# Performance work log

Measured on AMD Instinct MI355X. Metric: run time of the kernel, lower is better.

The kernel has to match this reference:

```python
import jax, jax.numpy as jnp
import numpy as np

BS, D_IN, D_H, D_Z = 4096, 784, 400, 20


def setup_inputs() -> dict:
    key = jax.random.key(0)
    ks = jax.random.split(key, 13)
    s = 0.05
    return {
        "x": jax.random.normal(ks[0], (BS, D_IN), dtype=jnp.float32),
        "W1": jax.random.normal(ks[1], (D_H, D_IN), dtype=jnp.float32) * s,
        "b1": jax.random.normal(ks[2], (D_H,), dtype=jnp.float32) * s,
        "W21": jax.random.normal(ks[3], (D_Z, D_H), dtype=jnp.float32) * s,
        "b21": jax.random.normal(ks[4], (D_Z,), dtype=jnp.float32) * s,
        "W22": jax.random.normal(ks[5], (D_Z, D_H), dtype=jnp.float32) * s,
        "b22": jax.random.normal(ks[6], (D_Z,), dtype=jnp.float32) * s,
        "W3": jax.random.normal(ks[7], (D_H, D_Z), dtype=jnp.float32) * s,
        "b3": jax.random.normal(ks[8], (D_H,), dtype=jnp.float32) * s,
        "W41": jax.random.normal(ks[9], (D_IN, D_H), dtype=jnp.float32) * s,
        "b41": jax.random.normal(ks[10], (D_IN,), dtype=jnp.float32) * s,
        "W42": jax.random.normal(ks[11], (D_IN, D_H), dtype=jnp.float32) * s,
        "b42": jax.random.normal(ks[12], (D_IN,), dtype=jnp.float32) * s,
    }


def reference(x, W1, b1, W21, b21, W22, b22, W3, b3, W41, b41, W42, b42):
    xr = x.reshape(-1, D_IN)                              # [bs, 784]
    # encode
    h1 = jax.nn.relu(xr @ W1.T + b1)                      # [bs, 400]
    mu = h1 @ W21.T + b21                                 # [bs, 20]
    logvar = h1 @ W22.T + b22                             # [bs, 20]
    # unscented sigma points: varsqrt[:, i] = sqrt(N)*logvar[:, i]*e_i
    N = D_Z
    sqrtN = jnp.asarray(np.sqrt(N), dtype=x.dtype)
    # delta[i, b, j] = sqrt(N) * logvar[b, i] * (i == j)   -> [N, bs, N]
    delta = sqrtN * logvar.T[:, :, None] * jnp.eye(N, dtype=x.dtype)[:, None, :]
    z = jnp.concatenate([mu[None] + delta, mu[None] - delta], axis=0)  # [2N, bs, N]

    def decode(zs):
        h3 = jax.nn.relu(zs @ W3.T + b3)                  # [bs, 400]
        return zs @ W41.T * 0 + (h3 @ W41.T + b41), h3 @ W42.T + b42

    def decode_clean(zs):
        h3 = jax.nn.relu(zs @ W3.T + b3)
        return h3 @ W41.T + b41, h3 @ W42.T + b42

    # original loop decodes every sigma point; recon_x keeps the last one
    mu_x, var_x = jax.vmap(decode_clean)(z)               # each [2N, bs, 784]
    recon_mu = mu_x[-1]
    recon_var = var_x[-1]
    return recon_mu, recon_var, mu, logvar, z
```

## Files before the change

kernel.cpp:

```cpp
#include <hip/hip_runtime.h>
#include <hip/hip_bf16.h>

#define BS   4096
#define DIN  784
#define DH   400
#define DZ   20

#define KP1  832
#define KPH  416
#define KPD  448

#define OFF_RMU  0
#define OFF_RVAR 3211264
#define OFF_MU   6422528
#define OFF_LV   6504448
#define OFF_Z    6586368

#define WS_WCAT  0
#define WS_W2C   1404928
#define WS_W1B   1444864
#define WS_H1B   2110464
#define WS_H3B   5518336

#define SQRT20F 4.47213595499958f

using short8 = __attribute__((ext_vector_type(8))) short;
using f4     = __attribute__((ext_vector_type(4))) float;
using i4     = __attribute__((ext_vector_type(4))) int;

__device__ __forceinline__ short bf16r(float f) {
    union { float f; unsigned u; } v; v.f = f;
    unsigned r = (v.u + 0x7fffu + ((v.u >> 16) & 1u)) >> 16;
    return (short)r;
}

__device__ __forceinline__ i4 pack8(const i4 q0, const i4 q1) {
    i4 d;
    d[0] = (q0[1] & 0xffff0000) | (int)(((unsigned)q0[0]) >> 16);
    d[1] = (q0[3] & 0xffff0000) | (int)(((unsigned)q0[2]) >> 16);
    d[2] = (q1[1] & 0xffff0000) | (int)(((unsigned)q1[0]) >> 16);
    d[3] = (q1[3] & 0xffff0000) | (int)(((unsigned)q1[2]) >> 16);
    return d;
}

__device__ __forceinline__ void glds16(const void* g, void* l) {
    __builtin_amdgcn_global_load_lds(
        (const __attribute__((address_space(1))) unsigned int*)g,
        (__attribute__((address_space(3))) unsigned int*)l,
        16, 0, 0);
}

__global__ void k0(const float* __restrict__ W1, const float* __restrict__ W41,
                   const float* __restrict__ W42, const float* __restrict__ W21,
                   const float* __restrict__ W22, char* __restrict__ ws) {
    const int N0 = 400 * 104;
    const int N1 = N0 + 1568 * 56;
    const int N2 = N1 + 48 * 52;
    int gid = blockIdx.x * 256 + threadIdx.x;
    if (gid >= N2) return;

    const float* sr = nullptr;
    short* dst;
    int c, DC;
    if (gid < N0) {
        int row = gid / 104; c = gid - row * 104; DC = 98;
        sr = W1 + (size_t)row * DIN;
        dst = (short*)(ws + WS_W1B) + (size_t)row * KP1 + c * 8;
    } else if (gid < N1) {
        int p = gid - N0;
        int row = p / 56; c = p - row * 56; DC = 50;
        sr = (row < 784) ? (W41 + (size_t)row * DH) : (W42 + (size_t)(row - 784) * DH);
        dst = (short*)(ws + WS_WCAT) + (size_t)row * KPD + c * 8;
    } else {
        int p = gid - N1;
        int row = p / 52; c = p - row * 52; DC = 50;
        if (row < 20)      sr = W21 + (size_t)row * DH;
        else if (row < 40) sr = W22 + (size_t)(row - 20) * DH;
        else               sr = nullptr;
        dst = (short*)(ws + WS_W2C) + (size_t)row * KPH + c * 8;
    }
    short8 v;
    if (c < DC && sr) {
        f4 a = *(const f4*)(sr + c * 8);
        f4 b = *(const f4*)(sr + c * 8 + 4);
#pragma unroll
        for (int e = 0; e < 4; ++e) { v[e] = bf16r(a[e]); v[4 + e] = bf16r(b[e]); }
    } else {
#pragma unroll
        for (int e = 0; e < 8; ++e) v[e] = 0;
    }
    *(short8*)dst = v;
}

__global__ __launch_bounds__(256)
void k1(const float* __restrict__ x, const float* __restrict__ b1,
        const short* __restrict__ W1b, short* __restrict__ h1b) {
    __shared__ short sA[2][64 * 64];
    __shared__ short sB[2][80 * 64];

    const int tid = threadIdx.x;
    const int bid = blockIdx.x;
    const int swz = (bid & 7) * 40 + (bid >> 3);
    const int bm = swz / 5, bn = swz - bm * 5;
    const int w = tid >> 6, l = tid & 63, lg = l >> 4, lr = l & 15;

    f4 acc[5] = {};
    i4 ar[4];

    auto a_load = [&](int kt) {
#pragma unroll
        for (int i = 0; i < 2; ++i) {
            int c = tid + i * 256;
            int row = c >> 3, kc = c & 7;
            int gk = kt * 64 + kc * 8;
            if (gk < DIN) {
                const i4* p = (const i4*)(x + (size_t)(bm * 64 + row) * DIN + gk);
                ar[2 * i] = p[0]; ar[2 * i + 1] = p[1];
            } else {
                ar[2 * i] = (i4){0, 0, 0, 0}; ar[2 * i + 1] = (i4){0, 0, 0, 0};
            }
        }
    };
    auto a_write = [&](int buf) {
#pragma unroll
        for (int i = 0; i < 2; ++i) {
            int c = tid + i * 256;
            int row = c >> 3, kc = c & 7;
            *(i4*)&sA[buf][(row * 8 + (kc ^ (row & 7))) * 8] = pack8(ar[2 * i], ar[2 * i + 1]);
        }
    };
    auto b_stage = [&](int buf, int kt) {
#pragma unroll
        for (int it = 0; it < 3; ++it) {
            int p = it * 256 + tid;
            if (p < 640) {
                int r = p >> 3, kc = (p & 7) ^ (r & 7);
                glds16(W1b + (size_t)(bn * 80 + r) * KP1 + kt * 64 + kc * 8, &sB[buf][p * 8]);
            }
        }
    };
    auto compute = [&](int buf) {
        const int row = w * 16 + lr;
#pragma unroll
        for (int kk = 0; kk < 2; ++kk) {
            short8 a = *(const short8*)&sA[buf][(row * 8 + ((kk * 4 + lg) ^ (row & 7))) * 8];
#pragma unroll
            for (int ni = 0; ni < 5; ++ni) {
                int brw = ni * 16 + lr;
                short8 b = *(const short8*)&sB[buf][(brw * 8 + ((kk * 4 + lg) ^ (brw & 7))) * 8];
                acc[ni] = __builtin_amdgcn_mfma_f32_16x16x32_bf16(a, b, acc[ni], 0, 0, 0);
            }
        }
    };

    a_load(0); b_stage(0, 0); a_write(0);
    __syncthreads();
    for (int kt = 0; kt < 13; ++kt) {
        const int cur = kt & 1;
        if (kt < 12) { a_load(kt + 1); b_stage(cur ^ 1, kt + 1); }
        compute(cur);
        if (kt < 12) a_write(cur ^ 1);
        __syncthreads();
    }

#pragma unroll
    for (int ni = 0; ni < 5; ++ni) {
        int col = bn * 80 + ni * 16 + lr;
        float bias = b1[col];
#pragma unroll
        for (int r = 0; r < 4; ++r) {
            int row = bm * 64 + w * 16 + lg * 4 + r;
            float v = acc[ni][r] + bias;
            h1b[(size_t)row * KPH + col] = bf16r(v > 0.f ? v : 0.f);
        }
    }
    if (bn == 4) {
        for (int p = tid; p < 64 * 16; p += 256) {
            int r = p >> 4, c = 400 + (p & 15);
            h1b[(size_t)(bm * 64 + r) * KPH + c] = 0;
        }
    }
}

__global__ __launch_bounds__(256)
void k_mid(const short* __restrict__ h1b, const short* __restrict__ w2c,
           const float* __restrict__ W3, const float* __restrict__ b3,
           const float* __restrict__ b21, const float* __restrict__ b22,
           float* __restrict__ out, short* __restrict__ h3b) {
    __shared__ short sA[16 * 416];
    __shared__ short sB[48 * 416];
    __shared__ short sW[400 * 40];
    __shared__ float muv[2][16][20];
    __shared__ short zl[16 * 40];
    __shared__ short h3s[16 * 448];

    const int tid = threadIdx.x;
    const int blk = blockIdx.x;
    const int w = tid >> 6, l = tid & 63, lg = l >> 4, lr = l & 15;
    const int r0 = blk * 16;

#pragma unroll
    for (int it = 0; it < 4; ++it) {
        int p = it * 256 + tid;
        if (p < 832) {
            int r = p / 52, cp = p - r * 52, c = cp ^ (r & 3);
            glds16(h1b + (size_t)(r0 + r) * KPH + c * 8, &sA[p * 8]);
        }
    }
#pragma unroll
    for (int it = 0; it < 10; ++it) {
        int p = it * 256 + tid;
        if (p < 2496) {
            int r = p / 52, cp = p - r * 52, c = cp ^ (r & 3);
            glds16(w2c + (size_t)r * KPH + c * 8, &sB[p * 8]);
        }
    }
    if (tid < 200) {
#pragma unroll
        for (int i = 0; i < 2; ++i) {
            int r = tid + i * 200;
            const float* src = W3 + (size_t)r * DZ;
            f4 f0 = *(const f4*)src;
            f4 f1 = *(const f4*)(src + 4);
            f4 f2 = *(const f4*)(src + 8);
            f4 f3 = *(const f4*)(src + 12);
            f4 f5 = *(const f4*)(src + 16);
            short8 c0, c1, c2, c3;
#pragma unroll
            for (int e = 0; e < 4; ++e) {
                c0[e] = bf16r(f0[e]); c0[4 + e] = bf16r(f1[e]);
                c1[e] = bf16r(f2[e]); c1[4 + e] = bf16r(f3[e]);
                c2[e] = bf16r(f5[e]); c2[4 + e] = 0;
                c3[e] = 0; c3[4 + e] = 0;
            }
            *(short8*)&sW[r * 40 + 0]  = c0;
            *(short8*)&sW[r * 40 + 8]  = c1;
            *(short8*)&sW[r * 40 + 16] = c2;
            *(short8*)&sW[r * 40 + 24] = c3;
        }
    }
    __syncthreads();

    if (w == 0) {
        f4 a3[3] = {};
#pragma unroll
        for (int kk = 0; kk < 13; ++kk) {
            short8 a = *(const short8*)&sA[(lr * 52 + ((kk * 4 + lg) ^ (lr & 3))) * 8];
#pragma unroll
            for (int ni = 0; ni < 3; ++ni) {
                int br = ni * 16 + lr;
                short8 b = *(const short8*)&sB[(br * 52 + ((kk * 4 + lg) ^ (br & 3))) * 8];
                a3[ni] = __builtin_amdgcn_mfma_f32_16x16x32_bf16(a, b, a3[ni], 0, 0, 0);
            }
        }
#pragma unroll
        for (int ni = 0; ni < 3; ++ni) {
            int n = ni * 16 + lr;
            if (n < 40) {
                float bias = (n < 20) ? b21[n] : b22[n - 20];
#pragma unroll
                for (int r = 0; r < 4; ++r) {
                    int row = lg * 4 + r;
                    float v = a3[ni][r] + bias;
                    if (n < 20) {
                        muv[0][row][n] = v;
                        out[OFF_MU + (size_t)(r0 + row) * 20 + n] = v;
                    } else {
                        muv[1][row][n - 20] = v;
                        out[OFF_LV + (size_t)(r0 + row) * 20 + (n - 20)] = v;
                    }
                }
            }
        }
    }
    __syncthreads();

    if (tid < 80) {
        int row = tid / 5, c = tid - (tid / 5) * 5;
        short8 v;
#pragma unroll
        for (int e = 0; e < 8; ++e) {
            int j = c * 8 + e;
            float val = 0.f;
            if (j < 20) {
                val = muv[0][row][j];
                if (j == 19) val -= SQRT20F * muv[1][row][19];
            }
            v[e] = bf16r(val);
        }
        *(short8*)&zl[row * 40 + c * 8] = v;
    } else if (tid < 176) {
        int t = tid - 80;
        int row = t / 6, c = t - (t / 6) * 6;
        short8 zz;
#pragma unroll
        for (int e = 0; e < 8; ++e) zz[e] = 0;
        *(short8*)&h3s[row * 448 + 400 + c * 8] = zz;
    }
    __syncthreads();

    for (int f = w; f < 25; f += 4) {
        int n0 = f * 16;
        short8 a = *(const short8*)&zl[lr * 40 + lg * 8];
        short8 b = *(const short8*)&sW[(n0 + lr) * 40 + lg * 8];
        f4 z4 = {};
        f4 accv = __builtin_amdgcn_mfma_f32_16x16x32_bf16(a, b, z4, 0, 0, 0);
        int n = n0 + lr;
        float bias = b3[n];
#pragma unroll
        for (int r = 0; r < 4; ++r) {
            int row = lg * 4 + r;
            float v = accv[r] + bias;
            h3s[row * 448 + n] = bf16r(v > 0.f ? v : 0.f);
        }
    }
    __syncthreads();

#pragma unroll
    for (int it = 0; it < 4; ++it) {
        int p = it * 256 + tid;
        if (p < 896) {
            int row = p / 56, c = p - (p / 56) * 56;
            *(short8*)(h3b + (size_t)(r0 + row) * KPD + c * 8) =
                *(const short8*)&h3s[row * 448 + c * 8];
        }
    }
}

__global__ __launch_bounds__(256)
void k_gemm4(const short* __restrict__ h3b, const short* __restrict__ wcat,
             const float* __restrict__ b41, const float* __restrict__ b42,
             float* __restrict__ out) {
    __shared__ short sA[2][128 * 64];
    __shared__ short sB[2][112 * 64];

    const int tid = threadIdx.x;
    const int bid = blockIdx.x;

    if (bid >= 448) {
        const int zb = bid - 448;
#pragma unroll 2
        for (int it = 0; it < 50; ++it) {
            int idx = it * 16384 + zb * 256 + tid;
            int s = idx / 20480;
            int rem = idx - s * 20480;
            int b = rem / 5, j4 = rem - b * 5;
            int sp = (s < 20) ? s : s - 20;
            f4 v = *(const f4*)(out + OFF_MU + (size_t)b * 20 + j4 * 4);
            if ((sp >> 2) == j4) {
                float add = ((s < 20) ? SQRT20F : -SQRT20F) * out[OFF_LV + (size_t)b * 20 + sp];
                int e = sp & 3;
#pragma unroll
                for (int k = 0; k < 4; ++k) v[k] += (e == k) ? add : 0.f;
            }
            *(f4*)(out + OFF_Z + (size_t)idx * 4) = v;
        }
        return;
    }

    const int swz = (bid & 7) * 56 + (bid >> 3);
    const int bm = swz / 14, bn = swz - bm * 14;
    const int w = tid >> 6, l = tid & 63, lg = l >> 4, lr = l & 15;

    f4 acc[2][7] = {};

    auto stage = [&](int buf, int kt) {
#pragma unroll
        for (int i = 0; i < 4; ++i) {
            int c = tid + i * 256;
            int r = c >> 3, kc = (c & 7) ^ (r & 7);
            glds16(h3b + (size_t)(bm * 128 + r) * KPD + kt * 64 + kc * 8, &sA[buf][c * 8]);
        }
#pragma unroll
        for (int i = 0; i < 4; ++i) {
            int c = tid + i * 256;
            if (c < 896) {
                int r = c >> 3, kc = (c & 7) ^ (r & 7);
                glds16(wcat + (size_t)(bn * 112 + r) * KPD + kt * 64 + kc * 8, &sB[buf][c * 8]);
            }
        }
    };

    stage(0, 0);
    __syncthreads();
    for (int kt = 0; kt < 7; ++kt) {
        const int cur = kt & 1;
        if (kt < 6) stage(cur ^ 1, kt + 1);
        const int row0 = w * 32 + lr, row1 = w * 32 + 16 + lr;
#pragma unroll
        for (int kk = 0; kk < 2; ++kk) {
            short8 a0 = *(const short8*)&sA[cur][(row0 * 8 + ((kk * 4 + lg) ^ (row0 & 7))) * 8];
            short8 a1 = *(const short8*)&sA[cur][(row1 * 8 + ((kk * 4 + lg) ^ (row1 & 7))) * 8];
#pragma unroll
            for (int ni = 0; ni < 7; ++ni) {
                int br = ni * 16 + lr;
                short8 b = *(const short8*)&sB[cur][(br * 8 + ((kk * 4 + lg) ^ (br & 7))) * 8];
                acc[0][ni] = __builtin_amdgcn_mfma_f32_16x16x32_bf16(a0, b, acc[0][ni], 0, 0, 0);
                acc[1][ni] = __builtin_amdgcn_mfma_f32_16x16x32_bf16(a1, b, acc[1][ni], 0, 0, 0);
            }
        }
        __syncthreads();
    }

    const bool first = (bn < 7);
#pragma unroll
    for (int mi = 0; mi < 2; ++mi)
#pragma unroll
        for (int ni = 0; ni < 7; ++ni) {
            int colt = bn * 112 + ni * 16 + lr;
            int cc = first ? colt : colt - 784;
            float bias = first ? b41[cc] : b42[cc];
            size_t base = first ? (size_t)OFF_RMU : (size_t)OFF_RVAR;
#pragma unroll
            for (int r = 0; r < 4; ++r) {
                size_t row = (size_t)(bm * 128 + w * 32 + mi * 16 + lg * 4 + r);
                out[base + row * DIN + cc] = acc[mi][ni][r] + bias;
            }
        }
}

extern "C" void kernel_launch(void* const* d_in, const int* in_sizes, int n_in,
                              void* d_out, int out_size, void* d_ws, size_t ws_size,
                              hipStream_t stream) {
    const float* x   = (const float*)d_in[0];
    const float* W1  = (const float*)d_in[1];
    const float* b1  = (const float*)d_in[2];
    const float* W21 = (const float*)d_in[3];
    const float* b21 = (const float*)d_in[4];
    const float* W22 = (const float*)d_in[5];
    const float* b22 = (const float*)d_in[6];
    const float* W3  = (const float*)d_in[7];
    const float* b3  = (const float*)d_in[8];
    const float* W41 = (const float*)d_in[9];
    const float* b41 = (const float*)d_in[10];
    const float* W42 = (const float*)d_in[11];
    const float* b42 = (const float*)d_in[12];

    float* out = (float*)d_out;
    char*  ws  = (char*)d_ws;
    const short* wcat = (const short*)(ws + WS_WCAT);
    const short* w2c  = (const short*)(ws + WS_W2C);
    const short* W1b  = (const short*)(ws + WS_W1B);
    short* h1b = (short*)(ws + WS_H1B);
    short* h3b = (short*)(ws + WS_H3B);

    k0<<<516, 256, 0, stream>>>(W1, W41, W42, W21, W22, ws);
    k1<<<320, 256, 0, stream>>>(x, b1, W1b, h1b);
    k_mid<<<256, 256, 0, stream>>>(h1b, w2c, W3, b3, b21, b22, out, h3b);
    k_gemm4<<<512, 256, 0, stream>>>(h3b, wcat, b41, b42, out);
}
```

Baseline: 51.78 us.

## Fuse four kernels into one persistent kernel with grid barriers and atomic tile queues

Replaces the four separate launches (weight conversion, first GEMM, middle encoder/decoder stage, final GEMM) with a single persistent kernel of 256 blocks × 512 threads. Stages are separated by a software grid barrier, and the two GEMM stages take tiles from atomic work counters. A memset resets the sync counters. The aim is to remove launch gaps and tail effects between kernels, at the cost of barrier spin overhead, one block per CU, and a dependence on all blocks being co-resident.

```diff
diff --git a/kernel.cpp b/kernel.cpp
--- a/kernel.cpp
+++ b/kernel.cpp
@@ -21,6 +21,7 @@
 #define WS_W1B   1444864
 #define WS_H1B   2110464
 #define WS_H3B   5518336
+#define WS_SYNC  9188352
 
 #define SQRT20F 4.47213595499958f
 
@@ -50,175 +51,205 @@
         16, 0, 0);
 }
 
-__global__ void k0(const float* __restrict__ W1, const float* __restrict__ W41,
-                   const float* __restrict__ W42, const float* __restrict__ W21,
-                   const float* __restrict__ W22, char* __restrict__ ws) {
-    const int N0 = 400 * 104;
-    const int N1 = N0 + 1568 * 56;
-    const int N2 = N1 + 48 * 52;
-    int gid = blockIdx.x * 256 + threadIdx.x;
-    if (gid >= N2) return;
-
-    const float* sr = nullptr;
-    short* dst;
-    int c, DC;
-    if (gid < N0) {
-        int row = gid / 104; c = gid - row * 104; DC = 98;
-        sr = W1 + (size_t)row * DIN;
-        dst = (short*)(ws + WS_W1B) + (size_t)row * KP1 + c * 8;
-    } else if (gid < N1) {
-        int p = gid - N0;
-        int row = p / 56; c = p - row * 56; DC = 50;
-        sr = (row < 784) ? (W41 + (size_t)row * DH) : (W42 + (size_t)(row - 784) * DH);
-        dst = (short*)(ws + WS_WCAT) + (size_t)row * KPD + c * 8;
-    } else {
-        int p = gid - N1;
-        int row = p / 52; c = p - row * 52; DC = 50;
-        if (row < 20)      sr = W21 + (size_t)row * DH;
-        else if (row < 40) sr = W22 + (size_t)(row - 20) * DH;
-        else               sr = nullptr;
-        dst = (short*)(ws + WS_W2C) + (size_t)row * KPH + c * 8;
+__device__ __forceinline__ void gridbar(unsigned* sync) {
+    __syncthreads();
+    if (threadIdx.x == 0) {
+        __threadfence();
+        unsigned g = atomicAdd(&sync[1], 0u);
+        if (atomicAdd(&sync[0], 1u) == 255u) {
+            atomicExch(&sync[0], 0u);
+            __threadfence();
+            atomicAdd(&sync[1], 1u);
+        } else {
+            while (atomicAdd(&sync[1], 0u) == g) __builtin_amdgcn_s_sleep(2);
+        }
+        __threadfence();
     }
-    short8 v;
-    if (c < DC && sr) {
-        f4 a = *(const f4*)(sr + c * 8);
-        f4 b = *(const f4*)(sr + c * 8 + 4);
-#pragma unroll
-        for (int e = 0; e < 4; ++e) { v[e] = bf16r(a[e]); v[4 + e] = bf16r(b[e]); }
-    } else {
-#pragma unroll
-        for (int e = 0; e < 8; ++e) v[e] = 0;
-    }
-    *(short8*)dst = v;
-}
-
-__global__ __launch_bounds__(256)
-void k1(const float* __restrict__ x, const float* __restrict__ b1,
-        const short* __restrict__ W1b, short* __restrict__ h1b) {
-    __shared__ short sA[2][64 * 64];
-    __shared__ short sB[2][80 * 64];
-
+    __syncthreads();
+}
+
+struct P1 { short sA[2][128 * 64]; short sB[2][80 * 64]; };
+struct P2 {
+    short sA[16 * 416]; short sB[48 * 416]; short sW[400 * 40];
+    float muv[2][16][20]; short zl[16 * 40]; short h3s[16 * 448];
+};
+struct P3 { short sA[2][128 * 64]; short sB[2][112 * 64]; };
+union SMem { P1 p1; P2 p2; P3 p3; };
+
+__global__ __launch_bounds__(512, 1)
+void fused(const float* __restrict__ x, const float* __restrict__ W1,
+           const float* __restrict__ b1,
+           const float* __restrict__ W21, const float* __restrict__ b21,
+           const float* __restrict__ W22, const float* __restrict__ b22,
+           const float* __restrict__ W3, const float* __restrict__ b3,
+           const float* __restrict__ W41, const float* __restrict__ b41,
+           const float* __restrict__ W42, const float* __restrict__ b42,
+           float* __restrict__ out, char* __restrict__ ws) {
+    __shared__ SMem sm;
+    __shared__ unsigned smt;
+
+    unsigned* sync = (unsigned*)(ws + WS_SYNC);
     const int tid = threadIdx.x;
     const int bid = blockIdx.x;
-    const int swz = (bid & 7) * 40 + (bid >> 3);
-    const int bm = swz / 5, bn = swz - bm * 5;
     const int w = tid >> 6, l = tid & 63, lg = l >> 4, lr = l & 15;
 
-    f4 acc[5] = {};
-    i4 ar[4];
-
-    auto a_load = [&](int kt) {
-#pragma unroll
-        for (int i = 0; i < 2; ++i) {
-            int c = tid + i * 256;
-            int row = c >> 3, kc = c & 7;
-            int gk = kt * 64 + kc * 8;
-            if (gk < DIN) {
-                const i4* p = (const i4*)(x + (size_t)(bm * 64 + row) * DIN + gk);
-                ar[2 * i] = p[0]; ar[2 * i + 1] = p[1];
+    short* w1b  = (short*)(ws + WS_W1B);
+    short* wcat = (short*)(ws + WS_WCAT);
+    short* w2c  = (short*)(ws + WS_W2C);
+    short* h1b  = (short*)(ws + WS_H1B);
+    short* h3b  = (short*)(ws + WS_H3B);
+
+    {
+        const int N0 = 400 * 104;
+        const int N1 = N0 + 1568 * 56;
+        const int N2 = N1 + 48 * 52;
+        for (int p = bid * 512 + tid; p < N2; p += 131072) {
+            const float* sr = nullptr;
+            short* dst;
+            int c, DC;
+            if (p < N0) {
+                int row = p / 104; c = p - row * 104; DC = 98;
+                sr = W1 + (size_t)row * DIN;
+                dst = w1b + (size_t)row * KP1 + c * 8;
+            } else if (p < N1) {
+                int q = p - N0;
+                int row = q / 56; c = q - row * 56; DC = 50;
+                sr = (row < 784) ? (W41 + (size_t)row * DH)
+                                 : (W42 + (size_t)(row - 784) * DH);
+                dst = wcat + (size_t)row * KPD + c * 8;
             } else {
-                ar[2 * i] = (i4){0, 0, 0, 0}; ar[2 * i + 1] = (i4){0, 0, 0, 0};
-            }
-        }
-    };
-    auto a_write = [&](int buf) {
-#pragma unroll
-        for (int i = 0; i < 2; ++i) {
-            int c = tid + i * 256;
-            int row = c >> 3, kc = c & 7;
-            *(i4*)&sA[buf][(row * 8 + (kc ^ (row & 7))) * 8] = pack8(ar[2 * i], ar[2 * i + 1]);
-        }
-    };
-    auto b_stage = [&](int buf, int kt) {
-#pragma unroll
-        for (int it = 0; it < 3; ++it) {
-            int p = it * 256 + tid;
-            if (p < 640) {
-                int r = p >> 3, kc = (p & 7) ^ (r & 7);
-                glds16(W1b + (size_t)(bn * 80 + r) * KP1 + kt * 64 + kc * 8, &sB[buf][p * 8]);
-            }
-        }
-    };
-    auto compute = [&](int buf) {
-        const int row = w * 16 + lr;
-#pragma unroll
-        for (int kk = 0; kk < 2; ++kk) {
-            short8 a = *(const short8*)&sA[buf][(row * 8 + ((kk * 4 + lg) ^ (row & 7))) * 8];
-#pragma unroll
-            for (int ni = 0; ni < 5; ++ni) {
-                int brw = ni * 16 + lr;
-                short8 b = *(const short8*)&sB[buf][(brw * 8 + ((kk * 4 + lg) ^ (brw & 7))) * 8];
-                acc[ni] = __builtin_amdgcn_mfma_f32_16x16x32_bf16(a, b, acc[ni], 0, 0, 0);
-            }
-        }
-    };
-
-    a_load(0); b_stage(0, 0); a_write(0);
-    __syncthreads();
-    for (int kt = 0; kt < 13; ++kt) {
-        const int cur = kt & 1;
-        if (kt < 12) { a_load(kt + 1); b_stage(cur ^ 1, kt + 1); }
-        compute(cur);
-        if (kt < 12) a_write(cur ^ 1);
-        __syncthreads();
+                int q = p - N1;
+                int row = q / 52; c = q - row * 52; DC = 50;
+                if (row < 20)      sr = W21 + (size_t)row * DH;
+                else if (row < 40) sr = W22 + (size_t)(row - 20) * DH;
+                else               sr = nullptr;
+                dst = w2c + (size_t)row * KPH + c * 8;
+            }
+            short8 v;
+            if (c < DC && sr) {
+                f4 a = *(const f4*)(sr + c * 8);
+                f4 b = *(const f4*)(sr + c * 8 + 4);
+#pragma unroll
+                for (int e = 0; e < 4; ++e) { v[e] = bf16r(a[e]); v[4 + e] = bf16r(b[e]); }
+            } else {
+#pragma unroll
+                for (int e = 0; e < 8; ++e) v[e] = 0;
+            }
+            *(short8*)dst = v;
+        }
     }
-
-#pragma unroll
-    for (int ni = 0; ni < 5; ++ni) {
-        int col = bn * 80 + ni * 16 + lr;
-        float bias = b1[col];
-#pragma unroll
-        for (int r = 0; r < 4; ++r) {
-            int row = bm * 64 + w * 16 + lg * 4 + r;
-            float v = acc[ni][r] + bias;
-            h1b[(size_t)row * KPH + col] = bf16r(v > 0.f ? v : 0.f);
+    gridbar(sync);
+
+    for (;;) {
+        if (tid == 0) smt = atomicAdd(&sync[2], 1u);
+        __syncthreads();
+        const unsigned t = smt;
+        __syncthreads();
+        if (t >= 160u) break;
+        const int swz = (t & 7) * 20 + (t >> 3);
+        const int bm = swz / 5, bn = swz - bm * 5;
+
+        f4 acc[5] = {};
+        i4 ar[4];
+
+        auto a_load = [&](int kt) {
+#pragma unroll
+            for (int i = 0; i < 2; ++i) {
+                int c = tid + i * 512;
+                int row = c >> 3, kc = c & 7;
+                int gk = kt * 64 + kc * 8;
+                if (gk < DIN) {
+                    const i4* p = (const i4*)(x + (size_t)(bm * 128 + row) * DIN + gk);
+                    ar[2 * i] = p[0]; ar[2 * i + 1] = p[1];
+                } else {
+                    ar[2 * i] = (i4){0, 0, 0, 0}; ar[2 * i + 1] = (i4){0, 0, 0, 0};
+                }
+            }
+        };
+        auto a_write = [&](int buf) {
+#pragma unroll
+            for (int i = 0; i < 2; ++i) {
+                int c = tid + i * 512;
+                int row = c >> 3, kc = c & 7;
+                *(i4*)&sm.p1.sA[buf][(row * 8 + (kc ^ (row & 7))) * 8] =
+                    pack8(ar[2 * i], ar[2 * i + 1]);
+            }
+        };
+        auto b_stage = [&](int buf, int kt) {
+#pragma unroll
+            for (int it = 0; it < 2; ++it) {
+                int p = it * 512 + tid;
+                if (p < 640) {
+                    int r = p >> 3, kc = (p & 7) ^ (r & 7);
+                    glds16(w1b + (size_t)(bn * 80 + r) * KP1 + kt * 64 + kc * 8,
+                           &sm.p1.sB[buf][p * 8]);
+                }
+            }
+        };
+        auto compute = [&](int buf) {
+            const int row = w * 16 + lr;
+#pragma unroll
+            for (int kk = 0; kk < 2; ++kk) {
+                short8 a = *(const short8*)&sm.p1.sA[buf][(row * 8 + ((kk * 4 + lg) ^ (row & 7))) * 8];
+#pragma unroll
+                for (int ni = 0; ni < 5; ++ni) {
+                    int brw = ni * 16 + lr;
+                    short8 b = *(const short8*)&sm.p1.sB[buf][(brw * 8 + ((kk * 4 + lg) ^ (brw & 7))) * 8];
+                    acc[ni] = __builtin_amdgcn_mfma_f32_16x16x32_bf16(a, b, acc[ni], 0, 0, 0);
+                }
+            }
+        };
+
+        a_load(0); b_stage(0, 0); a_write(0);
+        __syncthreads();
+        for (int kt = 0; kt < 13; ++kt) {
+            const int cur = kt & 1;
+            if (kt < 12) { a_load(kt + 1); b_stage(cur ^ 1, kt + 1); }
+            compute(cur);
+            if (kt < 12) a_write(cur ^ 1);
+            __syncthreads();
+        }
+
+#pragma unroll
+        for (int ni = 0; ni < 5; ++ni) {
+            int col = bn * 80 + ni * 16 + lr;
+            float bias = b1[col];
+#pragma unroll
+            for (int r = 0; r < 4; ++r) {
+                int row = bm * 128 + w * 16 + lg * 4 + r;
+                float v = acc[ni][r] + bias;
+                h1b[(size_t)row * KPH + col] = bf16r(v > 0.f ? v : 0.f);
+            }
+        }
+        if (bn == 4) {
+            for (int p = tid; p < 128 * 16; p += 512) {
+                int r = p >> 4, c = 400 + (p & 15);
+                h1b[(size_t)(bm * 128 + r) * KPH + c] = 0;
+            }
         }
     }
-    if (bn == 4) {
-        for (int p = tid; p < 64 * 16; p += 256) {
-            int r = p >> 4, c = 400 + (p & 15);
-            h1b[(size_t)(bm * 64 + r) * KPH + c] = 0;
-        }
-    }
-}
-
-__global__ __launch_bounds__(256)
-void k_mid(const short* __restrict__ h1b, const short* __restrict__ w2c,
-           const float* __restrict__ W3, const float* __restrict__ b3,
-           const float* __restrict__ b21, const float* __restrict__ b22,
-           float* __restrict__ out, short* __restrict__ h3b) {
-    __shared__ short sA[16 * 416];
-    __shared__ short sB[48 * 416];
-    __shared__ short sW[400 * 40];
-    __shared__ float muv[2][16][20];
-    __shared__ short zl[16 * 40];
-    __shared__ short h3s[16 * 448];
-
-    const int tid = threadIdx.x;
-    const int blk = blockIdx.x;
-    const int w = tid >> 6, l = tid & 63, lg = l >> 4, lr = l & 15;
-    const int r0 = blk * 16;
-
-#pragma unroll
-    for (int it = 0; it < 4; ++it) {
-        int p = it * 256 + tid;
-        if (p < 832) {
-            int r = p / 52, cp = p - r * 52, c = cp ^ (r & 3);
-            glds16(h1b + (size_t)(r0 + r) * KPH + c * 8, &sA[p * 8]);
-        }
-    }
-#pragma unroll
-    for (int it = 0; it < 10; ++it) {
-        int p = it * 256 + tid;
-        if (p < 2496) {
-            int r = p / 52, cp = p - r * 52, c = cp ^ (r & 3);
-            glds16(w2c + (size_t)r * KPH + c * 8, &sB[p * 8]);
-        }
-    }
-    if (tid < 200) {
-#pragma unroll
-        for (int i = 0; i < 2; ++i) {
-            int r = tid + i * 200;
+    gridbar(sync);
+
+    {
+        const int r0 = bid * 16;
+#pragma unroll
+        for (int it = 0; it < 2; ++it) {
+            int p = it * 512 + tid;
+            if (p < 832) {
+                int r = p / 52, cp = p - r * 52, c = cp ^ (r & 3);
+                glds16(h1b + (size_t)(r0 + r) * KPH + c * 8, &sm.p2.sA[p * 8]);
+            }
+        }
+#pragma unroll
+        for (int it = 0; it < 5; ++it) {
+            int p = it * 512 + tid;
+            if (p < 2496) {
+                int r = p / 52, cp = p - r * 52, c = cp ^ (r & 3);
+                glds16(w2c + (size_t)r * KPH + c * 8, &sm.p2.sB[p * 8]);
+            }
+        }
+        if (tid < 400) {
+            int r = tid;
             const float* src = W3 + (size_t)r * DZ;
             f4 f0 = *(const f4*)src;
             f4 f1 = *(const f4*)(src + 4);
@@ -233,178 +264,174 @@
                 c2[e] = bf16r(f5[e]); c2[4 + e] = 0;
                 c3[e] = 0; c3[4 + e] = 0;
             }
-            *(short8*)&sW[r * 40 + 0]  = c0;
-            *(short8*)&sW[r * 40 + 8]  = c1;
-            *(short8*)&sW[r * 40 + 16] = c2;
-            *(short8*)&sW[r * 40 + 24] = c3;
+            *(short8*)&sm.p2.sW[r * 40 + 0]  = c0;
+            *(short8*)&sm.p2.sW[r * 40 + 8]  = c1;
+            *(short8*)&sm.p2.sW[r * 40 + 16] = c2;
+            *(short8*)&sm.p2.sW[r * 40 + 24] = c3;
+        }
+        __syncthreads();
+
+        if (w == 0) {
+            f4 a3[3] = {};
+#pragma unroll
+            for (int kk = 0; kk < 13; ++kk) {
+                short8 a = *(const short8*)&sm.p2.sA[(lr * 52 + ((kk * 4 + lg) ^ (lr & 3))) * 8];
+#pragma unroll
+                for (int ni = 0; ni < 3; ++ni) {
+                    int br = ni * 16 + lr;
+                    short8 b = *(const short8*)&sm.p2.sB[(br * 52 + ((kk * 4 + lg) ^ (br & 3))) * 8];
+                    a3[ni] = __builtin_amdgcn_mfma_f32_16x16x32_bf16(a, b, a3[ni], 0, 0, 0);
+                }
+            }
+#pragma unroll
+            for (int ni = 0; ni < 3; ++ni) {
+                int n = ni * 16 + lr;
+                if (n < 40) {
+                    float bias = (n < 20) ? b21[n] : b22[n - 20];
+#pragma unroll
+                    for (int r = 0; r < 4; ++r) {
+                        int row = lg * 4 + r;
+                        float v = a3[ni][r] + bias;
+                        if (n < 20) {
+                            sm.p2.muv[0][row][n] = v;
+                            out[OFF_MU + (size_t)(r0 + row) * 20 + n] = v;
+                        } else {
+                            sm.p2.muv[1][row][n - 20] = v;
+                            out[OFF_LV + (size_t)(r0 + row) * 20 + (n - 20)] = v;
+                        }
+                    }
+                }
+            }
+        }
+        __syncthreads();
+
+        if (tid < 80) {
+            int row = tid / 5, c = tid - (tid / 5) * 5;
+            short8 v;
+#pragma unroll
+            for (int e = 0; e < 8; ++e) {
+                int j = c * 8 + e;
+                float val = 0.f;
+                if (j < 20) {
+                    val = sm.p2.muv[0][row][j];
+                    if (j == 19) val -= SQRT20F * sm.p2.muv[1][row][19];
+                }
+                v[e] = bf16r(val);
+            }
+            *(short8*)&sm.p2.zl[row * 40 + c * 8] = v;
+        } else if (tid < 176) {
+            int q = tid - 80;
+            int row = q / 6, c = q - (q / 6) * 6;
+            short8 zz;
+#pragma unroll
+            for (int e = 0; e < 8; ++e) zz[e] = 0;
+            *(short8*)&sm.p2.h3s[row * 448 + 400 + c * 8] = zz;
+        }
+        __syncthreads();
+
+        for (int f = w; f < 25; f += 8) {
+            int n0 = f * 16;
+            short8 a = *(const short8*)&sm.p2.zl[lr * 40 + lg * 8];
+            short8 b = *(const short8*)&sm.p2.sW[(n0 + lr) * 40 + lg * 8];
+            f4 z4 = {};
+            f4 accv = __builtin_amdgcn_mfma_f32_16x16x32_bf16(a, b, z4, 0, 0, 0);
+            int n = n0 + lr;
+            float bias = b3[n];
+#pragma unroll
+            for (int r = 0; r < 4; ++r) {
+                int row = lg * 4 + r;
+                float v = accv[r] + bias;
+                sm.p2.h3s[row * 448 + n] = bf16r(v > 0.f ? v : 0.f);
+            }
+        }
+        __syncthreads();
+
+#pragma unroll
+        for (int it = 0; it < 2; ++it) {
+            int p = it * 512 + tid;
+            if (p < 896) {
+                int row = p / 56, c = p - (p / 56) * 56;
+                *(short8*)(h3b + (size_t)(r0 + row) * KPD + c * 8) =
+                    *(const short8*)&sm.p2.h3s[row * 448 + c * 8];
+            }
         }
     }
-    __syncthreads();
-
-    if (w == 0) {
-        f4 a3[3] = {};
-#pragma unroll
-        for (int kk = 0; kk < 13; ++kk) {
-            short8 a = *(const short8*)&sA[(lr * 52 + ((kk * 4 + lg) ^ (lr & 3))) * 8];
-#pragma unroll
-            for (int ni = 0; ni < 3; ++ni) {
-                int br = ni * 16 + lr;
-                short8 b = *(const short8*)&sB[(br * 52 + ((kk * 4 + lg) ^ (br & 3))) * 8];
-                a3[ni] = __builtin_amdgcn_mfma_f32_16x16x32_bf16(a, b, a3[ni], 0, 0, 0);
-            }
-        }
-#pragma unroll
-        for (int ni = 0; ni < 3; ++ni) {
-            int n = ni * 16 + lr;
-            if (n < 40) {
-                float bias = (n < 20) ? b21[n] : b22[n - 20];
-#pragma unroll
-                for (int r = 0; r < 4; ++r) {
-                    int row = lg * 4 + r;
-                    float v = a3[ni][r] + bias;
-                    if (n < 20) {
-                        muv[0][row][n] = v;
-                        out[OFF_MU + (size_t)(r0 + row) * 20 + n] = v;
-                    } else {
-                        muv[1][row][n - 20] = v;
-                        out[OFF_LV + (size_t)(r0 + row) * 20 + (n - 20)] = v;
-                    }
-                }
-            }
-        }
-    }
-    __syncthreads();
-
-    if (tid < 80) {
-        int row = tid / 5, c = tid - (tid / 5) * 5;
-        short8 v;
-#pragma unroll
-        for (int e = 0; e < 8; ++e) {
-            int j = c * 8 + e;
-            float val = 0.f;
-            if (j < 20) {
-                val = muv[0][row][j];
-                if (j == 19) val -= SQRT20F * muv[1][row][19];
-            }
-            v[e] = bf16r(val);
-        }
-        *(short8*)&zl[row * 40 + c * 8] = v;
-    } else if (tid < 176) {
-        int t = tid - 80;
-        int row = t / 6, c = t - (t / 6) * 6;
-        short8 zz;
-#pragma unroll
-        for (int e = 0; e < 8; ++e) zz[e] = 0;
-        *(short8*)&h3s[row * 448 + 400 + c * 8] = zz;
-    }
-    __syncthreads();
-
-    for (int f = w; f < 25; f += 4) {
-        int n0 = f * 16;
-        short8 a = *(const short8*)&zl[lr * 40 + lg * 8];
-        short8 b = *(const short8*)&sW[(n0 + lr) * 40 + lg * 8];
-        f4 z4 = {};
-        f4 accv = __builtin_amdgcn_mfma_f32_16x16x32_bf16(a, b, z4, 0, 0, 0);
-        int n = n0 + lr;
-        float bias = b3[n];
-#pragma unroll
-        for (int r = 0; r < 4; ++r) {
-            int row = lg * 4 + r;
-            float v = accv[r] + bias;
-            h3s[row * 448 + n] = bf16r(v > 0.f ? v : 0.f);
-        }
-    }
-    __syncthreads();
-
-#pragma unroll
-    for (int it = 0; it < 4; ++it) {
-        int p = it * 256 + tid;
-        if (p < 896) {
-            int row = p / 56, c = p - (p / 56) * 56;
-            *(short8*)(h3b + (size_t)(r0 + row) * KPD + c * 8) =
-                *(const short8*)&h3s[row * 448 + c * 8];
-        }
-    }
-}
-
-__global__ __launch_bounds__(256)
-void k_gemm4(const short* __restrict__ h3b, const short* __restrict__ wcat,
-             const float* __restrict__ b41, const float* __restrict__ b42,
-             float* __restrict__ out) {
-    __shared__ short sA[2][128 * 64];
-    __shared__ short sB[2][112 * 64];
-
-    const int tid = threadIdx.x;
-    const int bid = blockIdx.x;
-
-    if (bid >= 448) {
-        const int zb = bid - 448;
-#pragma unroll 2
-        for (int it = 0; it < 50; ++it) {
-            int idx = it * 16384 + zb * 256 + tid;
-            int s = idx / 20480;
-            int rem = idx - s * 20480;
-            int b = rem / 5, j4 = rem - b * 5;
-            int sp = (s < 20) ? s : s - 20;
-            f4 v = *(const f4*)(out + OFF_MU + (size_t)b * 20 + j4 * 4);
-            if ((sp >> 2) == j4) {
-                float add = ((s < 20) ? SQRT20F : -SQRT20F) * out[OFF_LV + (size_t)b * 20 + sp];
-                int e = sp & 3;
-#pragma unroll
-                for (int k = 0; k < 4; ++k) v[k] += (e == k) ? add : 0.f;
-            }
-            *(f4*)(out + OFF_Z + (size_t)idx * 4) = v;
-        }
-        return;
-    }
-
-    const int swz = (bid & 7) * 56 + (bid >> 3);
-    const int bm = swz / 14, bn = swz - bm * 14;
-    const int w = tid >> 6, l = tid & 63, lg = l >> 4, lr = l & 15;
-
-    f4 acc[2][7] = {};
-
-    auto stage = [&](int buf, int kt) {
-#pragma unroll
-        for (int i = 0; i < 4; ++i) {
-            int c = tid + i * 256;
-            int r = c >> 3, kc = (c & 7) ^ (r & 7);
-            glds16(h3b + (size_t)(bm * 128 + r) * KPD + kt * 64 + kc * 8, &sA[buf][c * 8]);
-        }
-#pragma unroll
-        for (int i = 0; i < 4; ++i) {
-            int c = tid + i * 256;
-            if (c < 896) {
+    gridbar(sync);
+
+    for (;;) {
+        if (tid == 0) smt = atomicAdd(&sync[3], 1u);
+        __syncthreads();
+        const unsigned t = smt;
+        __syncthreads();
+        if (t >= 512u) break;
+
+        if (t < 64u) {
+            const int zb = (int)t;
+#pragma unroll 5
+            for (int it = 0; it < 25; ++it) {
+                int idx = it * 32768 + zb * 512 + tid;
+                int s = idx / 20480;
+                int rem = idx - s * 20480;
+                int b = rem / 5, j4 = rem - b * 5;
+                int sp = (s < 20) ? s : s - 20;
+                f4 v = *(const f4*)(out + OFF_MU + (size_t)b * 20 + j4 * 4);
+                if ((sp >> 2) == j4) {
+                    float add = ((s < 20) ? SQRT20F : -SQRT20F) *
+                                out[OFF_LV + (size_t)b * 20 + sp];
+                    int e = sp & 3;
+#pragma unroll
+                    for (int k = 0; k < 4; ++k) v[k] += (e == k) ? add : 0.f;
+                }
+                *(f4*)(out + OFF_Z + (size_t)idx * 4) = v;
+            }
+            continue;
+        }
+
+        const int g = (int)t - 64;
+        const int swz = (g & 7) * 56 + (g >> 3);
+        const int bm = swz / 14, bn = swz - bm * 14;
+
+        f4 acc[7] = {};
+
+        auto stage = [&](int buf, int kt) {
+#pragma unroll
+            for (int i = 0; i < 2; ++i) {
+                int c = tid + i * 512;
                 int r = c >> 3, kc = (c & 7) ^ (r & 7);
-                glds16(wcat + (size_t)(bn * 112 + r) * KPD + kt * 64 + kc * 8, &sB[buf][c * 8]);
-            }
-        }
-    };
-
-    stage(0, 0);
-    __syncthreads();
-    for (int kt = 0; kt < 7; ++kt) {
-        const int cur = kt & 1;
-        if (kt < 6) stage(cur ^ 1, kt + 1);
-        const int row0 = w * 32 + lr, row1 = w * 32 + 16 + lr;
-#pragma unroll
-        for (int kk = 0; kk < 2; ++kk) {
-            short8 a0 = *(const short8*)&sA[cur][(row0 * 8 + ((kk * 4 + lg) ^ (row0 & 7))) * 8];
-            short8 a1 = *(const short8*)&sA[cur][(row1 * 8 + ((kk * 4 + lg) ^ (row1 & 7))) * 8];
-#pragma unroll
-            for (int ni = 0; ni < 7; ++ni) {
-                int br = ni * 16 + lr;
-                short8 b = *(const short8*)&sB[cur][(br * 8 + ((kk * 4 + lg) ^ (br & 7))) * 8];
-                acc[0][ni] = __builtin_amdgcn_mfma_f32_16x16x32_bf16(a0, b, acc[0][ni], 0, 0, 0);
-                acc[1][ni] = __builtin_amdgcn_mfma_f32_16x16x32_bf16(a1, b, acc[1][ni], 0, 0, 0);
-            }
-        }
-        __syncthreads();
-    }
-
-    const bool first = (bn < 7);
-#pragma unroll
-    for (int mi = 0; mi < 2; ++mi)
+                glds16(h3b + (size_t)(bm * 128 + r) * KPD + kt * 64 + kc * 8,
+                       &sm.p3.sA[buf][c * 8]);
+            }
+#pragma unroll
+            for (int i = 0; i < 2; ++i) {
+                int c = tid + i * 512;
+                if (c < 896) {
+                    int r = c >> 3, kc = (c & 7) ^ (r & 7);
+                    glds16(wcat + (size_t)(bn * 112 + r) * KPD + kt * 64 + kc * 8,
+                           &sm.p3.sB[buf][c * 8]);
+                }
+            }
+        };
+
+        stage(0, 0);
+        __syncthreads();
+        for (int kt = 0; kt < 7; ++kt) {
+            const int cur = kt & 1;
+            if (kt < 6) stage(cur ^ 1, kt + 1);
+            const int row = w * 16 + lr;
+#pragma unroll
+            for (int kk = 0; kk < 2; ++kk) {
+                short8 a = *(const short8*)&sm.p3.sA[cur][(row * 8 + ((kk * 4 + lg) ^ (row & 7))) * 8];
+#pragma unroll
+                for (int ni = 0; ni < 7; ++ni) {
+                    int br = ni * 16 + lr;
+                    short8 b = *(const short8*)&sm.p3.sB[cur][(br * 8 + ((kk * 4 + lg) ^ (br & 7))) * 8];
+                    acc[ni] = __builtin_amdgcn_mfma_f32_16x16x32_bf16(a, b, acc[ni], 0, 0, 0);
+                }
+            }
+            __syncthreads();
+        }
+
+        const bool first = (bn < 7);
 #pragma unroll
         for (int ni = 0; ni < 7; ++ni) {
             int colt = bn * 112 + ni * 16 + lr;
@@ -413,10 +440,11 @@
             size_t base = first ? (size_t)OFF_RMU : (size_t)OFF_RVAR;
 #pragma unroll
             for (int r = 0; r < 4; ++r) {
-                size_t row = (size_t)(bm * 128 + w * 32 + mi * 16 + lg * 4 + r);
-                out[base + row * DIN + cc] = acc[mi][ni][r] + bias;
-            }
-        }
+                size_t row = (size_t)(bm * 128 + w * 16 + lg * 4 + r);
+                out[base + row * DIN + cc] = acc[ni][r] + bias;
+            }
+        }
+    }
 }
 
 extern "C" void kernel_launch(void* const* d_in, const int* in_sizes, int n_in,
@@ -438,14 +466,8 @@
 
     float* out = (float*)d_out;
     char*  ws  = (char*)d_ws;
-    const short* wcat = (const short*)(ws + WS_WCAT);
-    const short* w2c  = (const short*)(ws + WS_W2C);
-    const short* W1b  = (const short*)(ws + WS_W1B);
-    short* h1b = (short*)(ws + WS_H1B);
-    short* h3b = (short*)(ws + WS_H3B);
-
-    k0<<<516, 256, 0, stream>>>(W1, W41, W42, W21, W22, ws);
-    k1<<<320, 256, 0, stream>>>(x, b1, W1b, h1b);
-    k_mid<<<256, 256, 0, stream>>>(h1b, w2c, W3, b3, b21, b22, out, h3b);
-    k_gemm4<<<512, 256, 0, stream>>>(h3b, wcat, b41, b42, out);
-}
+
+    hipMemsetAsync(ws + WS_SYNC, 0, 64, stream);
+    fused<<<256, 512, 0, stream>>>(x, W1, b1, W21, b21, W22, b22,
+                                   W3, b3, W41, b41, W42, b42, out, ws);
+}
```

After: 169.3 us. +227.0%, slower.
